# Optimization experiments

Hardware: AMD Instinct MI355X
Metric: run time of the kernel (lower is better)

## Reference

```python
import jax, jax.numpy as jnp
import numpy as np

NUM_HEADS = 16
EMBED_DIM = 1024

def setup_inputs() -> dict:
    key = jax.random.key(0)
    k1, k2, k3 = jax.random.split(key, 3)
    x = jax.random.normal(k1, (4, 2048, EMBED_DIM), dtype=jnp.float32)
    # Linear weights (lecun-style scaling for numerical sanity)
    w_qkv = jax.random.normal(k2, (EMBED_DIM, 3 * EMBED_DIM), dtype=jnp.float32) / np.sqrt(EMBED_DIM)
    w_out = jax.random.normal(k3, (EMBED_DIM, EMBED_DIM), dtype=jnp.float32) / np.sqrt(EMBED_DIM)
    return {"x": x, "w_qkv": w_qkv, "w_out": w_out}

def reference(x, w_qkv, w_out):
    b, s, d = x.shape
    h = NUM_HEADS
    dh = d // h
    qkv = x @ w_qkv                        # [b, s, 3d]
    q, k, v = jnp.split(qkv, 3, axis=-1)   # each [b, s, d]
    def split_heads(t):
        return t.reshape(b, s, h, dh).transpose(0, 2, 1, 3)  # [b, h, s, dh]
    q, k, v = split_heads(q), split_heads(k), split_heads(v)
    logits = jnp.einsum('bhsd,bhtd->bhst', q, k) / jnp.sqrt(jnp.asarray(dh, q.dtype))
    weights = jax.nn.softmax(logits, axis=-1)
    out = jnp.einsum('bhst,bhtd->bhsd', weights, v)
    out = out.transpose(0, 2, 1, 3).reshape(b, s, d)  # [b, s, d]
    return out @ w_out
```

## Files before the change

kernel.cpp:

```cpp
#include <hip/hip_runtime.h>
#include <hip/hip_bf16.h>
#include <math.h>

typedef unsigned short u16;
typedef unsigned long long u64;
typedef __attribute__((ext_vector_type(8))) short short8;
typedef __attribute__((ext_vector_type(4))) float floatx4;

#define BB 4
#define SS 2048
#define DD 1024
#define HH 16
#define DHH 64
#define BSZ (BB*SS)

__device__ inline u16 bf1(float f) {
  return (u16)((__float_as_uint(f) + 0x8000u) >> 16);
}
__device__ inline unsigned pk2bf(float a, float b) {
  return __builtin_amdgcn_perm(__float_as_uint(b) + 0x8000u,
                               __float_as_uint(a) + 0x8000u, 0x07060302u);
}
__device__ inline unsigned pkbf(float a, float b) {
  unsigned r;
  asm("v_cvt_pk_bf16_f32 %0, %1, %2" : "=v"(r) : "v"(a), "v"(b));
  return r;
}

__device__ inline short8 ld16(const u16* p) {
  union { uint4 u; short8 s; } cv;
  cv.u = *(const uint4*)p;
  return cv.s;
}

__device__ inline void gload_lds16(const u16* g, u16* l) {
  __builtin_amdgcn_global_load_lds(
      (const __attribute__((address_space(1))) void*)g,
      (__attribute__((address_space(3))) void*)l, 16, 0, 0);
}

__device__ inline void swap_qpair(unsigned &a, unsigned &b) {
  asm("v_permlane32_swap_b32 %0, %1" : "+v"(a), "+v"(b));
  asm("v_permlane16_swap_b32 %0, %1" : "+v"(a), "+v"(b));
}

#define VMCNT(n) asm volatile("s_waitcnt vmcnt(" #n ")" ::: "memory")

__global__ __launch_bounds__(256) void cvt_f32_bf16(
    const float* __restrict__ in, u16* __restrict__ out) {
  int t = blockIdx.x * 256 + threadIdx.x;
  const float4* p = (const float4*)in + (size_t)t * 2;
  float4 a = p[0], b = p[1];
  uint4 r;
  r.x = pk2bf(a.x, a.y); r.y = pk2bf(a.z, a.w);
  r.z = pk2bf(b.x, b.y); r.w = pk2bf(b.z, b.w);
  *((uint4*)out + t) = r;
}

__global__ __launch_bounds__(256) void transpose_f32_bf16(
    const float* __restrict__ in, u16* __restrict__ out, int K, int N) {
  __shared__ u16 tile[32][33];
  int k0 = blockIdx.y * 32, n0 = blockIdx.x * 32;
  int tx = threadIdx.x, ty = threadIdx.y;
  #pragma unroll
  for (int i = 0; i < 32; i += 8)
    tile[ty + i][tx] = bf1(in[(size_t)(k0 + ty + i) * N + n0 + tx]);
  __syncthreads();
  #pragma unroll
  for (int i = 0; i < 32; i += 8)
    out[(size_t)(n0 + ty + i) * K + k0 + tx] = tile[tx][ty + i];
}

__global__ __launch_bounds__(512, 2) void gemm8p_nt(
    const u16* __restrict__ A, const u16* __restrict__ Bt, int K,
    u16* __restrict__ q, u16* __restrict__ kk, u16* __restrict__ vv) {
  __shared__ __attribute__((aligned(16))) u16 sh[65536];
  const int tid = threadIdx.x;
  const int lane = tid & 63, wave = tid >> 6;
  const int col = lane & 15, quad = lane >> 4;
  const int wm = (wave >> 2) * 128;
  const int wn = (wave & 3) * 64;
  const int nbx = gridDim.x;
  const int nwg = nbx * gridDim.y;
  const int lin = blockIdx.y * nbx + blockIdx.x;
  const int swz = (lin & 7) * (nwg >> 3) + (lin >> 3);
  const int m0 = (swz / nbx) * 256, n0 = (swz % nbx) * 256;

  floatx4 acc[8][4];
  #pragma unroll
  for (int i = 0; i < 8; i++)
    #pragma unroll
    for (int j = 0; j < 4; j++) acc[i][j] = (floatx4){0.f, 0.f, 0.f, 0.f};

  const int srow = tid & 255, sg = tid >> 8;
  const u16* ga = A + (size_t)(m0 + srow) * K + sg * 8;
  const u16* gb = Bt + (size_t)(n0 + srow) * K + sg * 8;
  u16* lw = sh + wave * 512;

  #define STG(mat, gbase, db, ks, tk) do {                                   \
    gload_lds16(gbase + (tk)*64 + (ks)*32,                                   \
                lw + (db)*32768 + (mat)*16384 + (ks)*8192);                  \
    gload_lds16(gbase + (tk)*64 + (ks)*32 + 16,                              \
                lw + (db)*32768 + (mat)*16384 + (ks)*8192 + 4096);           \
  } while (0)

  const int NT = K >> 6;
  STG(0, ga, 0, 0, 0);
  STG(1, gb, 0, 0, 0);
  STG(0, ga, 0, 1, 0);
  STG(1, gb, 0, 1, 0);

  for (int tk = 0; tk < NT; ++tk) {
    const int db = tk & 1;
    const u16* Ab = sh + db * 32768;
    const u16* Bb = sh + db * 32768 + 16384;
    const bool more = (tk + 1) < NT;
    short8 af[8], b0, b1;

    VMCNT(4);
    __builtin_amdgcn_s_barrier();
    __builtin_amdgcn_sched_barrier(0);
    if (more) STG(0, ga, db ^ 1, 0, tk + 1);
    #pragma unroll
    for (int mf = 0; mf < 8; mf++)
      af[mf] = ld16(Ab + quad * 2048 + (wm + mf * 16 + col) * 8);
    b0 = ld16(Bb + quad * 2048 + (wn + col) * 8);
    b1 = ld16(Bb + quad * 2048 + (wn + 16 + col) * 8);
    __builtin_amdgcn_s_setprio(1);
    #pragma unroll
    for (int mf = 0; mf < 8; mf++) {
      acc[mf][0] = __builtin_amdgcn_mfma_f32_16x16x32_bf16(af[mf], b0, acc[mf][0], 0, 0, 0);
      acc[mf][1] = __builtin_amdgcn_mfma_f32_16x16x32_bf16(af[mf], b1, acc[mf][1], 0, 0, 0);
    }
    __builtin_amdgcn_s_setprio(0);

    if (more) STG(1, gb, db ^ 1, 0, tk + 1);
    b0 = ld16(Bb + quad * 2048 + (wn + 32 + col) * 8);
    b1 = ld16(Bb + quad * 2048 + (wn + 48 + col) * 8);
    __builtin_amdgcn_s_setprio(1);
    #pragma unroll
    for (int mf = 0; mf < 8; mf++) {
      acc[mf][2] = __builtin_amdgcn_mfma_f32_16x16x32_bf16(af[mf], b0, acc[mf][2], 0, 0, 0);
      acc[mf][3] = __builtin_amdgcn_mfma_f32_16x16x32_bf16(af[mf], b1, acc[mf][3], 0, 0, 0);
    }
    __builtin_amdgcn_s_setprio(0);

    if (tk == NT - 1) { VMCNT(0); } else { VMCNT(4); }
    __builtin_amdgcn_s_barrier();
    __builtin_amdgcn_sched_barrier(0);
    if (more) STG(0, ga, db ^ 1, 1, tk + 1);
    #pragma unroll
    for (int mf = 0; mf < 8; mf++)
      af[mf] = ld16(Ab + 8192 + quad * 2048 + (wm + mf * 16 + col) * 8);
    b0 = ld16(Bb + 8192 + quad * 2048 + (wn + col) * 8);
    b1 = ld16(Bb + 8192 + quad * 2048 + (wn + 16 + col) * 8);
    __builtin_amdgcn_s_setprio(1);
    #pragma unroll
    for (int mf = 0; mf < 8; mf++) {
      acc[mf][0] = __builtin_amdgcn_mfma_f32_16x16x32_bf16(af[mf], b0, acc[mf][0], 0, 0, 0);
      acc[mf][1] = __builtin_amdgcn_mfma_f32_16x16x32_bf16(af[mf], b1, acc[mf][1], 0, 0, 0);
    }
    __builtin_amdgcn_s_setprio(0);

    if (more) STG(1, gb, db ^ 1, 1, tk + 1);
    b0 = ld16(Bb + 8192 + quad * 2048 + (wn + 32 + col) * 8);
    b1 = ld16(Bb + 8192 + quad * 2048 + (wn + 48 + col) * 8);
    __builtin_amdgcn_s_setprio(1);
    #pragma unroll
    for (int mf = 0; mf < 8; mf++) {
      acc[mf][2] = __builtin_amdgcn_mfma_f32_16x16x32_bf16(af[mf], b0, acc[mf][2], 0, 0, 0);
      acc[mf][3] = __builtin_amdgcn_mfma_f32_16x16x32_bf16(af[mf], b1, acc[mf][3], 0, 0, 0);
    }
    __builtin_amdgcn_s_setprio(0);
  }
  #undef STG

  #pragma unroll
  for (int mf = 0; mf < 8; mf++) {
    #pragma unroll
    for (int nf = 0; nf < 4; nf++) {
      int gm0 = m0 + wm + mf * 16 + quad * 4;
      int gn = n0 + wn + nf * 16 + col;
      int which = gn >> 10;
      if (which == 2) {
        int dh = gn & 63, hh = (gn >> 6) & 15;
        int bb2 = gm0 >> 11, s = gm0 & 2047;
        uint2 pk;
        pk.x = pk2bf(acc[mf][nf][0], acc[mf][nf][1]);
        pk.y = pk2bf(acc[mf][nf][2], acc[mf][nf][3]);
        *(uint2*)(vv + ((size_t)((bb2 * HH + hh) * 64 + dh)) * SS + s) = pk;
      } else {
        int f = gn & 1023;
        u16* dst = (which == 0) ? q : kk;
        float sc = (which == 0) ? 0.18033688f : 1.0f;
        #pragma unroll
        for (int r = 0; r < 4; r++)
          dst[(size_t)(gm0 + r) * DD + f] = bf1(acc[mf][nf][r] * sc);
      }
    }
  }
}

template <int MODE>
__global__ __launch_bounds__(256) void gemm_nt(
    const u16* __restrict__ A, const u16* __restrict__ Bt,
    int M, int N, int K,
    float* __restrict__ outf, u16* __restrict__ q, u16* __restrict__ kk,
    u16* __restrict__ vv) {
  __shared__ __attribute__((aligned(16))) u16 As[128 * 32];
  __shared__ __attribute__((aligned(16))) u16 Bs[128 * 32];
  const int tid = threadIdx.x;
  const int lane = tid & 63;
  const int wave = tid >> 6;
  const int col = lane & 15, quad = lane >> 4;
  const int nbx = gridDim.x;
  const int nwg = nbx * gridDim.y;
  const int lin = blockIdx.y * nbx + blockIdx.x;
  const int swz = (lin & 7) * (nwg >> 3) + (lin >> 3);
  const int m0 = (swz / nbx) * 128, n0 = (swz % nbx) * 128;
  const int wm = (wave & 1) * 64, wn = (wave >> 1) * 64;

  floatx4 acc[4][4];
  #pragma unroll
  for (int i = 0; i < 4; i++)
    #pragma unroll
    for (int j = 0; j < 4; j++) acc[i][j] = (floatx4){0.f, 0.f, 0.f, 0.f};

  const u16* ga0 = A + (size_t)(m0 + (tid >> 2)) * K + (tid & 3) * 8;
  const u16* ga1 = ga0 + (size_t)64 * K;
  const u16* gb0 = Bt + (size_t)(n0 + (tid >> 2)) * K + (tid & 3) * 8;
  const u16* gb1 = gb0 + (size_t)64 * K;
  u16* lA0 = As + wave * 512;
  u16* lB0 = Bs + wave * 512;

  for (int kb = 0; kb < K; kb += 32) {
    __syncthreads();
    gload_lds16(ga0 + kb, lA0);
    gload_lds16(ga1 + kb, lA0 + 2048);
    gload_lds16(gb0 + kb, lB0);
    gload_lds16(gb1 + kb, lB0 + 2048);
    __syncthreads();
    short8 af[4], bfr[4];
    #pragma unroll
    for (int i = 0; i < 4; i++)
      af[i] = ld16(As + (wm + i * 16 + col) * 32 + quad * 8);
    #pragma unroll
    for (int i = 0; i < 4; i++)
      bfr[i] = ld16(Bs + (wn + i * 16 + col) * 32 + quad * 8);
    #pragma unroll
    for (int i = 0; i < 4; i++)
      #pragma unroll
      for (int j = 0; j < 4; j++)
        acc[i][j] = __builtin_amdgcn_mfma_f32_16x16x32_bf16(af[i], bfr[j],
                                                            acc[i][j], 0, 0, 0);
  }

  #pragma unroll
  for (int i = 0; i < 4; i++) {
    #pragma unroll
    for (int j = 0; j < 4; j++) {
      int gm0 = m0 + wm + i * 16 + quad * 4;
      int gn = n0 + wn + j * 16 + col;
      if (MODE == 0) {
        #pragma unroll
        for (int r = 0; r < 4; r++)
          outf[(size_t)(gm0 + r) * N + gn] = acc[i][j][r];
      } else {
        int which = gn >> 10;
        if (which == 2) {
          int dh = gn & 63, hh = (gn >> 6) & 15;
          int bb = gm0 >> 11, s = gm0 & 2047;
          uint2 pk;
          pk.x = pk2bf(acc[i][j][0], acc[i][j][1]);
          pk.y = pk2bf(acc[i][j][2], acc[i][j][3]);
          *(uint2*)(vv + ((size_t)((bb * HH + hh) * 64 + dh)) * SS + s) = pk;
        } else {
          int f = gn & 1023;
          u16* dst = (which == 0) ? q : kk;
          float sc = (which == 0) ? 0.18033688f : 1.0f;
          #pragma unroll
          for (int r = 0; r < 4; r++)
            dst[(size_t)(gm0 + r) * DD + f] = bf1(acc[i][j][r] * sc);
        }
      }
    }
  }
}

__global__ __launch_bounds__(256, 2) void attn_kernel(
    const u16* __restrict__ Q, const u16* __restrict__ K,
    const u16* __restrict__ VT, u16* __restrict__ O) {
  __shared__ __attribute__((aligned(16))) u16 Ks[64 * 72];
  __shared__ __attribute__((aligned(16))) u16 Vs[64 * 72];

  const int tid = threadIdx.x, lane = tid & 63, wave = tid >> 6;
  const int col = lane & 15, quad = lane >> 4;
  const int bid = blockIdx.x;
  const int idx = ((bid & 7) << 6) + (bid >> 3);
  const int qt = idx & 7;
  const int h = (idx >> 3) & 15;
  const int b = idx >> 7;

  const size_t rowbase = (size_t)b * SS;
  const int qrow0 = qt * 256 + wave * 64;

  short8 qf[4][2];
  #pragma unroll
  for (int qs = 0; qs < 4; qs++)
    #pragma unroll
    for (int kc = 0; kc < 2; kc++)
      qf[qs][kc] = ld16(Q + (rowbase + qrow0 + qs * 16 + col) * DD + h * DHH +
                        kc * 32 + quad * 8);

  const u16* kg = K + rowbase * DD + h * DHH;
  const u16* vg = VT + (size_t)(b * HH + h) * DHH * SS;

  union { unsigned u[4]; short8 s8; } onesf;
  {
    unsigned ow = (col == 0) ? 0x3F803F80u : 0u;
    onesf.u[0] = ow; onesf.u[1] = ow; onesf.u[2] = ow; onesf.u[3] = ow;
  }

  floatx4 o[4][5];
  #pragma unroll
  for (int qs = 0; qs < 4; qs++)
    #pragma unroll
    for (int mt = 0; mt < 5; mt++) o[qs][mt] = (floatx4){0.f, 0.f, 0.f, 0.f};

  const int srow = tid >> 2, sc = (tid & 3) * 16;

  uint4 k0 = *(const uint4*)(kg + (size_t)srow * DD + sc);
  uint4 k1 = *(const uint4*)(kg + (size_t)srow * DD + sc + 8);
  uint4 v0 = *(const uint4*)(vg + (size_t)srow * SS + sc);
  uint4 v1 = *(const uint4*)(vg + (size_t)srow * SS + sc + 8);

  for (int kt = 0; kt < SS; kt += 64) {
    __syncthreads();
    *(uint4*)(Ks + srow * 72 + sc) = k0;
    *(uint4*)(Ks + srow * 72 + sc + 8) = k1;
    *(uint4*)(Vs + srow * 72 + sc) = v0;
    *(uint4*)(Vs + srow * 72 + sc + 8) = v1;
    __syncthreads();

    if (kt + 64 < SS) {
      k0 = *(const uint4*)(kg + (size_t)(kt + 64 + srow) * DD + sc);
      k1 = *(const uint4*)(kg + (size_t)(kt + 64 + srow) * DD + sc + 8);
      v0 = *(const uint4*)(vg + (size_t)srow * SS + kt + 64 + sc);
      v1 = *(const uint4*)(vg + (size_t)srow * SS + kt + 64 + sc + 8);
    }

    #pragma unroll
    for (int h2 = 0; h2 < 2; h2++) {
      unsigned pk[4][2][2];
      #pragma unroll
      for (int mtl = 0; mtl < 2; mtl++) {
        const int mt = h2 * 2 + mtl;
        short8 kf0 = ld16(Ks + (mt * 16 + col) * 72 + quad * 8);
        short8 kf1 = ld16(Ks + (mt * 16 + col) * 72 + 32 + quad * 8);
        #pragma unroll
        for (int qs = 0; qs < 4; qs++) {
          floatx4 s = (floatx4){0.f, 0.f, 0.f, 0.f};
          __builtin_amdgcn_s_setprio(1);
          s = __builtin_amdgcn_mfma_f32_16x16x32_bf16(kf0, qf[qs][0], s, 0, 0, 0);
          s = __builtin_amdgcn_mfma_f32_16x16x32_bf16(kf1, qf[qs][1], s, 0, 0, 0);
          __builtin_amdgcn_s_setprio(0);
          pk[qs][mtl][0] =
              pkbf(__builtin_amdgcn_exp2f(s[0]), __builtin_amdgcn_exp2f(s[1]));
          pk[qs][mtl][1] =
              pkbf(__builtin_amdgcn_exp2f(s[2]), __builtin_amdgcn_exp2f(s[3]));
        }
      }
      short8 va[4];
      #pragma unroll
      for (int mt5 = 0; mt5 < 4; mt5++)
        va[mt5] = ld16(Vs + (mt5 * 16 + col) * 72 + h2 * 32 + quad * 8);
      #pragma unroll
      for (int qs = 0; qs < 4; qs++) {
        unsigned wa = pk[qs][0][0], wb = pk[qs][1][0];
        swap_qpair(wa, wb);
        unsigned wc = pk[qs][0][1], wd = pk[qs][1][1];
        swap_qpair(wc, wd);
        union { unsigned u[4]; short8 s8; } bb;
        bb.u[0] = wa; bb.u[1] = wc; bb.u[2] = wb; bb.u[3] = wd;
        __builtin_amdgcn_s_setprio(1);
        #pragma unroll
        for (int mt5 = 0; mt5 < 4; mt5++)
          o[qs][mt5] = __builtin_amdgcn_mfma_f32_16x16x32_bf16(
              va[mt5], bb.s8, o[qs][mt5], 0, 0, 0);
        o[qs][4] = __builtin_amdgcn_mfma_f32_16x16x32_bf16(
            onesf.s8, bb.s8, o[qs][4], 0, 0, 0);
        __builtin_amdgcn_s_setprio(0);
      }
    }
  }

  #pragma unroll
  for (int qs = 0; qs < 4; qs++) {
    float l = __shfl(o[qs][4][0], col, 64);
    float inv = 1.0f / l;
    u16* ob = O + (rowbase + qrow0 + qs * 16 + col) * DD + h * DHH;
    #pragma unroll
    for (int mt = 0; mt < 4; mt++) {
      uint2 pk;
      pk.x = pkbf(o[qs][mt][0] * inv, o[qs][mt][1] * inv);
      pk.y = pkbf(o[qs][mt][2] * inv, o[qs][mt][3] * inv);
      *(uint2*)(ob + mt * 16 + quad * 4) = pk;
    }
  }
}

extern "C" void kernel_launch(void* const* d_in, const int* in_sizes, int n_in,
                              void* d_out, int out_size, void* d_ws,
                              size_t ws_size, hipStream_t stream) {
  const float* x = (const float*)d_in[0];
  const float* w_qkv = (const float*)d_in[1];
  const float* w_out = (const float*)d_in[2];
  float* out = (float*)d_out;

  u16* ws = (u16*)d_ws;
  u16* wT = ws;
  u16* q = wT + (size_t)3072 * 1024;
  u16* vt = q + (size_t)BSZ * DD;
  u16* k = (u16*)d_out;
  u16* xb = k + (size_t)BSZ * DD;
  u16* att = q;

  cvt_f32_bf16<<<dim3(BSZ * DD / (256 * 8)), 256, 0, stream>>>(x, xb);
  transpose_f32_bf16<<<dim3(3072 / 32, 1024 / 32), dim3(32, 8), 0, stream>>>(
      w_qkv, wT, 1024, 3072);
  gemm8p_nt<<<dim3(3072 / 256, BSZ / 256), 512, 0, stream>>>(
      xb, wT, 1024, q, k, vt);
  transpose_f32_bf16<<<dim3(1024 / 32, 1024 / 32), dim3(32, 8), 0, stream>>>(
      w_out, wT, 1024, 1024);
  attn_kernel<<<dim3(BB * HH * (SS / 256)), 256, 0, stream>>>(q, k, vt, att);
  gemm_nt<0><<<dim3(1024 / 128, BSZ / 128), 256, 0, stream>>>(
      att, wT, BSZ, 1024, 1024, out, nullptr, nullptr, nullptr);
}
```

Baseline: 301.3 us.

## Merge input prep kernels and deepen QKV GEMM global-to-LDS prefetch pipeline

The fp32-to-bf16 conversion of x and the w_qkv transpose now run as one kernel launch, which removes a launch and its tail gap. The QKV GEMM main loop is restructured so that loads for the next K tiles are issued at finer granularity, up to two tiles ahead. Extra barriers around each MFMA phase keep the shared buffers safe, and K is hard-coded as a compile-time constant. This aims to hide more global-memory latency, at the cost of more barriers and a tighter vmcnt dependency scheme that is easy to get wrong.

```diff
diff --git a/kernel.cpp b/kernel.cpp
--- a/kernel.cpp
+++ b/kernel.cpp
@@ -46,15 +46,32 @@
 
 #define VMCNT(n) asm volatile("s_waitcnt vmcnt(" #n ")" ::: "memory")
 
-__global__ __launch_bounds__(256) void cvt_f32_bf16(
-    const float* __restrict__ in, u16* __restrict__ out) {
-  int t = blockIdx.x * 256 + threadIdx.x;
-  const float4* p = (const float4*)in + (size_t)t * 2;
-  float4 a = p[0], b = p[1];
-  uint4 r;
-  r.x = pk2bf(a.x, a.y); r.y = pk2bf(a.z, a.w);
-  r.z = pk2bf(b.x, b.y); r.w = pk2bf(b.z, b.w);
-  *((uint4*)out + t) = r;
+__global__ __launch_bounds__(256) void prep_kernel(
+    const float* __restrict__ x, u16* __restrict__ xb,
+    const float* __restrict__ w_qkv, u16* __restrict__ wT) {
+  __shared__ u16 tile[32][33];
+  const int bid = blockIdx.x, tid = threadIdx.x;
+  if (bid < 4096) {
+    int t = bid * 256 + tid;
+    const float4* p = (const float4*)x + (size_t)t * 2;
+    float4 a = p[0], b = p[1];
+    uint4 r;
+    r.x = pk2bf(a.x, a.y); r.y = pk2bf(a.z, a.w);
+    r.z = pk2bf(b.x, b.y); r.w = pk2bf(b.z, b.w);
+    *((uint4*)xb + t) = r;
+  } else {
+    const int local = bid - 4096;
+    const int K = 1024, N = 3072;
+    int n0 = (local % 96) * 32, k0 = (local / 96) * 32;
+    int tx = tid & 31, ty = tid >> 5;
+    #pragma unroll
+    for (int i = 0; i < 32; i += 8)
+      tile[ty + i][tx] = bf1(w_qkv[(size_t)(k0 + ty + i) * N + n0 + tx]);
+    __syncthreads();
+    #pragma unroll
+    for (int i = 0; i < 32; i += 8)
+      wT[(size_t)(n0 + ty + i) * K + k0 + tx] = tile[tx][ty + i];
+  }
 }
 
 __global__ __launch_bounds__(256) void transpose_f32_bf16(
@@ -72,8 +89,9 @@
 }
 
 __global__ __launch_bounds__(512, 2) void gemm8p_nt(
-    const u16* __restrict__ A, const u16* __restrict__ Bt, int K,
+    const u16* __restrict__ A, const u16* __restrict__ Bt,
     u16* __restrict__ q, u16* __restrict__ kk, u16* __restrict__ vv) {
+  const int K = 1024, NT = 16;
   __shared__ __attribute__((aligned(16))) u16 sh[65536];
   const int tid = threadIdx.x;
   const int lane = tid & 63, wave = tid >> 6;
@@ -92,40 +110,39 @@
     #pragma unroll
     for (int j = 0; j < 4; j++) acc[i][j] = (floatx4){0.f, 0.f, 0.f, 0.f};
 
-  const int srow = tid & 255, sg = tid >> 8;
-  const u16* ga = A + (size_t)(m0 + srow) * K + sg * 8;
-  const u16* gb = Bt + (size_t)(n0 + srow) * K + sg * 8;
+  const int sr = tid & 255, sg = tid >> 8;
+  const u16* gaS = A + (size_t)(m0 + sr) * K + sg * 8;
+  const u16* gbS = Bt + (size_t)(n0 + sr) * K + sg * 8;
   u16* lw = sh + wave * 512;
 
-  #define STG(mat, gbase, db, ks, tk) do {                                   \
-    gload_lds16(gbase + (tk)*64 + (ks)*32,                                   \
-                lw + (db)*32768 + (mat)*16384 + (ks)*8192);                  \
-    gload_lds16(gbase + (tk)*64 + (ks)*32 + 16,                              \
-                lw + (db)*32768 + (mat)*16384 + (ks)*8192 + 4096);           \
+  #define STG(matPtr, matIdx, kh, t) do {                                    \
+    gload_lds16(matPtr + (t) * 64 + (kh) * 32,                               \
+                lw + ((t) & 1) * 32768 + (matIdx) * 16384 + (kh) * 8192);    \
+    gload_lds16(matPtr + (t) * 64 + (kh) * 32 + 16,                          \
+                lw + ((t) & 1) * 32768 + (matIdx) * 16384 + (kh) * 8192 +    \
+                    4096);                                                   \
   } while (0)
 
-  const int NT = K >> 6;
-  STG(0, ga, 0, 0, 0);
-  STG(1, gb, 0, 0, 0);
-  STG(0, ga, 0, 1, 0);
-  STG(1, gb, 0, 1, 0);
-
-  for (int tk = 0; tk < NT; ++tk) {
-    const int db = tk & 1;
+  STG(gaS, 0, 0, 0); STG(gbS, 1, 0, 0); STG(gaS, 0, 1, 0); STG(gbS, 1, 1, 0);
+  STG(gaS, 0, 0, 1); STG(gbS, 1, 0, 1); STG(gaS, 0, 1, 1);
+  VMCNT(6);
+  __builtin_amdgcn_s_barrier();
+
+  short8 af[8], b0, b1;
+  #pragma unroll 1
+  for (int t = 0; t < NT; ++t) {
+    const int db = t & 1;
     const u16* Ab = sh + db * 32768;
     const u16* Bb = sh + db * 32768 + 16384;
-    const bool more = (tk + 1) < NT;
-    short8 af[8], b0, b1;
-
-    VMCNT(4);
-    __builtin_amdgcn_s_barrier();
-    __builtin_amdgcn_sched_barrier(0);
-    if (more) STG(0, ga, db ^ 1, 0, tk + 1);
+
     #pragma unroll
     for (int mf = 0; mf < 8; mf++)
       af[mf] = ld16(Ab + quad * 2048 + (wm + mf * 16 + col) * 8);
     b0 = ld16(Bb + quad * 2048 + (wn + col) * 8);
     b1 = ld16(Bb + quad * 2048 + (wn + 16 + col) * 8);
+    if (t + 1 < NT) STG(gbS, 1, 1, t + 1);
+    __builtin_amdgcn_sched_barrier(0);
+    __builtin_amdgcn_s_barrier();
     __builtin_amdgcn_s_setprio(1);
     #pragma unroll
     for (int mf = 0; mf < 8; mf++) {
@@ -133,10 +150,13 @@
       acc[mf][1] = __builtin_amdgcn_mfma_f32_16x16x32_bf16(af[mf], b1, acc[mf][1], 0, 0, 0);
     }
     __builtin_amdgcn_s_setprio(0);
-
-    if (more) STG(1, gb, db ^ 1, 0, tk + 1);
+    __builtin_amdgcn_s_barrier();
+
     b0 = ld16(Bb + quad * 2048 + (wn + 32 + col) * 8);
     b1 = ld16(Bb + quad * 2048 + (wn + 48 + col) * 8);
+    if (t + 2 < NT) STG(gaS, 0, 0, t + 2);
+    __builtin_amdgcn_sched_barrier(0);
+    __builtin_amdgcn_s_barrier();
     __builtin_amdgcn_s_setprio(1);
     #pragma unroll
     for (int mf = 0; mf < 8; mf++) {
@@ -144,16 +164,16 @@
       acc[mf][3] = __builtin_amdgcn_mfma_f32_16x16x32_bf16(af[mf], b1, acc[mf][3], 0, 0, 0);
     }
     __builtin_amdgcn_s_setprio(0);
-
-    if (tk == NT - 1) { VMCNT(0); } else { VMCNT(4); }
-    __builtin_amdgcn_s_barrier();
-    __builtin_amdgcn_sched_barrier(0);
-    if (more) STG(0, ga, db ^ 1, 1, tk + 1);
+    __builtin_amdgcn_s_barrier();
+
     #pragma unroll
     for (int mf = 0; mf < 8; mf++)
       af[mf] = ld16(Ab + 8192 + quad * 2048 + (wm + mf * 16 + col) * 8);
     b0 = ld16(Bb + 8192 + quad * 2048 + (wn + col) * 8);
     b1 = ld16(Bb + 8192 + quad * 2048 + (wn + 16 + col) * 8);
+    if (t + 2 < NT) STG(gbS, 1, 0, t + 2);
+    __builtin_amdgcn_sched_barrier(0);
+    __builtin_amdgcn_s_barrier();
     __builtin_amdgcn_s_setprio(1);
     #pragma unroll
     for (int mf = 0; mf < 8; mf++) {
@@ -161,10 +181,13 @@
       acc[mf][1] = __builtin_amdgcn_mfma_f32_16x16x32_bf16(af[mf], b1, acc[mf][1], 0, 0, 0);
     }
     __builtin_amdgcn_s_setprio(0);
-
-    if (more) STG(1, gb, db ^ 1, 1, tk + 1);
+    __builtin_amdgcn_s_barrier();
+
     b0 = ld16(Bb + 8192 + quad * 2048 + (wn + 32 + col) * 8);
     b1 = ld16(Bb + 8192 + quad * 2048 + (wn + 48 + col) * 8);
+    if (t + 2 < NT) STG(gaS, 0, 1, t + 2);
+    __builtin_amdgcn_sched_barrier(0);
+    __builtin_amdgcn_s_barrier();
     __builtin_amdgcn_s_setprio(1);
     #pragma unroll
     for (int mf = 0; mf < 8; mf++) {
@@ -172,6 +195,8 @@
       acc[mf][3] = __builtin_amdgcn_mfma_f32_16x16x32_bf16(af[mf], b1, acc[mf][3], 0, 0, 0);
     }
     __builtin_amdgcn_s_setprio(0);
+    if (t + 1 < NT) { if (t + 2 < NT) { VMCNT(6); } else { VMCNT(0); } }
+    __builtin_amdgcn_s_barrier();
   }
   #undef STG
 
@@ -425,11 +450,9 @@
   u16* xb = k + (size_t)BSZ * DD;
   u16* att = q;
 
-  cvt_f32_bf16<<<dim3(BSZ * DD / (256 * 8)), 256, 0, stream>>>(x, xb);
-  transpose_f32_bf16<<<dim3(3072 / 32, 1024 / 32), dim3(32, 8), 0, stream>>>(
-      w_qkv, wT, 1024, 3072);
+  prep_kernel<<<dim3(4096 + 3072), 256, 0, stream>>>(x, xb, w_qkv, wT);
   gemm8p_nt<<<dim3(3072 / 256, BSZ / 256), 512, 0, stream>>>(
-      xb, wT, 1024, q, k, vt);
+      xb, wT, q, k, vt);
   transpose_f32_bf16<<<dim3(1024 / 32, 1024 / 32), dim3(32, 8), 0, stream>>>(
       w_out, wT, 1024, 1024);
   attn_kernel<<<dim3(BB * HH * (SS / 256)), 256, 0, stream>>>(q, k, vt, att);
```

New measurement: 282.7 us. 1.07x faster.
